# Kernel optimization log

Hardware: AMD Instinct MI355X
Metric: run time of the kernel (lower is better)

Reference implementation:

```python
import jax, jax.numpy as jnp
import numpy as np

R, STEPS, INJECT = 8, 4, 0.1


def _rmsnorm(v, w, eps=1e-6):
    return v * jax.lax.rsqrt(jnp.mean(v * v, axis=-1, keepdims=True) + eps) * w


def _layernorm(v, eps=1e-5):
    m = jnp.mean(v, axis=-1, keepdims=True)
    c = v - m
    return c * jax.lax.rsqrt(jnp.mean(c * c, axis=-1, keepdims=True) + eps)


def setup_inputs() -> dict:
    key = jax.random.key(0)
    ks = jax.random.split(key, 32)
    D, H, B, L = 1024, 256, 32, 2048
    s = 0.02
    inp = {
        'x': jax.random.normal(ks[0], (B, L, D), jnp.float32),
        'u': jax.random.uniform(ks[1], (STEPS, B, 16), jnp.float32),
        'W_e1': s * jax.random.normal(ks[2], (D, H)), 'b_e1': jnp.zeros((H,)),
        'W_e2': s * jax.random.normal(ks[3], (H, R * D)), 'b_e2': jnp.zeros((R * D,)),
        'W_ih': s * jax.random.normal(ks[4], (D + R * D, 3 * H)), 'b_ih': jnp.zeros((3 * H,)),
        'W_hh': s * jax.random.normal(ks[5], (H, 3 * H)), 'b_hh': jnp.zeros((3 * H,)),
        'ctrl_h0': jnp.zeros((H,)),
        'W_op': s * jax.random.normal(ks[6], (H, 16)), 'b_op': jnp.zeros((16,)),
        'W_src': s * jax.random.normal(ks[7], (H, R)), 'b_src': jnp.zeros((R,)),
        'W_dst': s * jax.random.normal(ks[8], (H, R)), 'b_dst': jnp.zeros((R,)),
        'W_aux': s * jax.random.normal(ks[9], (H, R)), 'b_aux': jnp.zeros((R,)),
        'W_proj': s * jax.random.normal(ks[10], (D, D)),
        'op_scale': jnp.ones((1,)),
        'Wv': s * jax.random.normal(ks[11], (D, D)), 'bv': jnp.zeros((D,)),
        'Wo': s * jax.random.normal(ks[12], (D, D)), 'bo': jnp.zeros((D,)),
        'W_d1': s * jax.random.normal(ks[13], (R * D, H)), 'b_d1': jnp.zeros((H,)),
        'W_d2': s * jax.random.normal(ks[14], (H, D)), 'b_d2': jnp.zeros((D,)),
        'norm_w': jnp.ones((D,)),
    }
    return inp


def reference(x, u, W_e1, b_e1, W_e2, b_e2, W_ih, b_ih, W_hh, b_hh, ctrl_h0,
              W_op, b_op, W_src, b_src, W_dst, b_dst, W_aux, b_aux,
              W_proj, op_scale, Wv, bv, Wo, bo, W_d1, b_d1, W_d2, b_d2, norm_w):
    B, L, D = x.shape
    pooled = x.mean(1)                                             # [B,D]
    regs = (jax.nn.gelu(pooled @ W_e1 + b_e1, approximate=False) @ W_e2 + b_e2).reshape(B, R, D)
    h = jnp.broadcast_to(ctrl_h0, (B, ctrl_h0.shape[0]))
    halt = jnp.zeros((B, 1), x.dtype)
    gumbel = -jnp.log(-jnp.log(u + 1e-20) + 1e-20)                 # [STEPS,B,16]
    op_trace = []
    for s in range(STEPS):
        ci = jnp.concatenate([pooled, regs.reshape(B, -1)], -1)    # [B, D+R*D]
        gi = ci @ W_ih + b_ih
        gh = h @ W_hh + b_hh
        ir, iz, inn = jnp.split(gi, 3, -1)
        hr, hz, hn = jnp.split(gh, 3, -1)
        r = jax.nn.sigmoid(ir + hr)
        z = jax.nn.sigmoid(iz + hz)
        n = jnp.tanh(inn + r * hn)
        h = (1.0 - z) * n + z * h                                  # GRUCell
        op_w = jax.nn.softmax(h @ W_op + b_op + gumbel[s], -1)     # gumbel-softmax, tau=1, soft
        src_w = jax.nn.softmax(h @ W_src + b_src, -1)
        dst_w = jax.nn.softmax(h @ W_dst + b_dst, -1)
        aux_w = jax.nn.softmax(h @ W_aux + b_aux, -1)
        src = jnp.einsum('br,brd->bd', src_w, regs)
        dst = jnp.einsum('br,brd->bd', dst_w, regs)
        aux = jnp.einsum('br,brd->bd', aux_w, regs)
        halt = halt + op_w[:, 15:16]
        live = jnp.clip(1.0 - halt, 0.0, None)
        # seq-len-1 MHA: softmax over one key == 1 -> out_proj(v_proj(aux))
        attn_out = (aux @ Wv + bv) @ Wo + bo
        results = jnp.stack([
            dst,                               # 0 NOP
            dst + src,                         # 1 ADD
            jax.nn.sigmoid(src) * dst,         # 2 GATE
            _layernorm(src),                   # 3 NORM
            src @ W_proj,                      # 4 PROJ
            src + dst,                         # 5 RESIDUAL
            attn_out,                          # 6 ATTEND
            -src,                              # 7 NEGATE
            src * op_scale,                    # 8 SCALE
            src,                               # 9 SWAP (as written)
            jnp.maximum(src, dst),             # 10 MAX
            jnp.minimum(src, dst),             # 11 MIN
            jax.nn.relu(src),                  # 12 RELU
            jnp.tanh(src),                     # 13 TANH
            (src * dst) @ W_proj,              # 14 OUTER
            dst,                               # 15 HALT
        ], axis=1)                             # [B,16,D]
        result = jnp.einsum('bo,bod->bd', op_w, results)
        regs = regs + dst_w[:, :, None] * (result * live)[:, None, :]
        op_trace.append(jnp.argmax(op_w, -1))
    prog_out = jax.nn.gelu(regs.reshape(B, -1) @ W_d1 + b_d1, approximate=False) @ W_d2 + b_d2
    prog_out = _rmsnorm(prog_out, norm_w)
    x_prog = _rmsnorm(x + prog_out[:, None, :] * INJECT, norm_w)
    return x_prog, regs, prog_out, jnp.stack(op_trace, axis=1)
```

## Files before the change

### kernel.cpp

```cpp
#include <hip/hip_runtime.h>
#include <math.h>
#include <stddef.h>

#define BB 32
#define LL 2048
#define DD 1024
#define HH 256
#define NSTEPS 4
#define RD 8192
#define G3 768

#define OUT_REGS 67108864UL
#define OUT_PO   67371008UL
#define OUT_TR   67403776UL

#define MM_KC 128
#define ATS 516

__device__ __forceinline__ float sigf(float x){ return 1.0f/(1.0f+expf(-x)); }
__device__ __forceinline__ float geluf(float x){ return x*0.5f*(1.0f+erff(x*0.70710678118654752f)); }

union SMem {
  struct { float At[8*ATS]; float Wt[MM_KC*64]; } mm;
  struct { float A[64*68]; float B[64*64]; } w2;
  struct { float hnew[HH]; float logit[40]; float wsm[40]; } ctl;
  struct { float ow[16]; float dw[8]; float redS[4]; float redQ[4]; float stats[2]; } comb;
  struct { float d1[HH]; float redQ[4]; float stats[1]; } dec;
};

struct MegaP {
  const float *x, *u, *W_e1, *b_e1, *W_e2, *b_e2, *W_ih, *b_ih, *W_hh, *b_hh, *h0;
  const float *W_op, *b_op, *W_src, *b_src, *W_dst, *b_dst, *W_aux, *b_aux;
  const float *W_proj, *op_sc, *Wv, *bv, *Wo, *bo, *W_d1, *b_d1, *W_d2, *b_d2, *norm_w;
  float *pool_part, *pooled, *e1, *regs, *gip_part, *gi_part, *ghpart, *hbuf, *halt;
  float *opw, *dstw, *live, *srcv, *dstv, *tvec, *avec, *p8a, *p10, *d1part, *pn;
  float *W2, *bvWo;
  float *out;
};

__device__ void st_mm2(SMem& sm, const float* __restrict__ in, int in_ld,
                       const float* __restrict__ W, int row_off, int ldw,
                       float* __restrict__ part, int nb, int layer, int nk, int t){
  float acc[16];
  #pragma unroll
  for (int i=0;i<16;++i) acc[i]=0.f;
  const int n0 = nb*64;
  for (int c=0;c<nk;++c){
    const int k0 = (layer*nk + c)*MM_KC;
    __syncthreads();
    if (t < 128){
      #pragma unroll
      for (int rep=0; rep<8; ++rep){
        int idx = t + rep*128;
        int b = idx & 31, k4 = idx >> 5;
        float4 g = *(const float4*)(in + (size_t)b*in_ld + k0 + k4*4);
        float* a = sm.mm.At + (b>>2)*ATS + k4*16 + (b&3);
        a[0]=g.x; a[4]=g.y; a[8]=g.z; a[12]=g.w;
      }
      #pragma unroll
      for (int rep=0; rep<16; ++rep){
        int idx = t + rep*128;
        int k = idx >> 4, nq4 = idx & 15;
        *(float4*)(sm.mm.Wt + k*64 + nq4*4) =
          *(const float4*)(W + (size_t)(row_off + k0 + k)*ldw + n0 + nq4*4);
      }
    }
    __syncthreads();
    if (t < 128){
      const int nq = t & 15, bq = t >> 4;
      const float4* A4 = (const float4*)sm.mm.At + bq*129;
      const float4* W4 = (const float4*)sm.mm.Wt + nq;
      #pragma unroll 4
      for (int kk=0; kk<MM_KC; ++kk){
        float4 a = A4[kk];
        float4 w = W4[kk*16];
        acc[0] +=a.x*w.x; acc[1] +=a.x*w.y; acc[2] +=a.x*w.z; acc[3] +=a.x*w.w;
        acc[4] +=a.y*w.x; acc[5] +=a.y*w.y; acc[6] +=a.y*w.z; acc[7] +=a.y*w.w;
        acc[8] +=a.z*w.x; acc[9] +=a.z*w.y; acc[10]+=a.z*w.z; acc[11]+=a.z*w.w;
        acc[12]+=a.w*w.x; acc[13]+=a.w*w.y; acc[14]+=a.w*w.z; acc[15]+=a.w*w.w;
      }
    }
  }
  if (t < 128){
    const int nq = t & 15, bq = t >> 4;
    float* pp = part + (size_t)(layer*32 + bq*4)*ldw + n0 + nq*4;
    #pragma unroll
    for (int i=0;i<4;++i){
      float4 o; o.x=acc[i*4]; o.y=acc[i*4+1]; o.z=acc[i*4+2]; o.w=acc[i*4+3];
      *(float4*)(pp + (size_t)i*ldw) = o;
    }
  }
}

__device__ void st_w2(SMem& sm, const MegaP& P, int blk, int t){
  const int r0 = (blk>>4)*64, n0 = (blk&15)*64;
  const int tr = t>>4, tc = t&15;
  float4 acc[4];
  acc[0]=make_float4(0,0,0,0); acc[1]=make_float4(0,0,0,0);
  acc[2]=make_float4(0,0,0,0); acc[3]=make_float4(0,0,0,0);
  for (int kc=0; kc<16; ++kc){
    const int k0 = kc*64;
    __syncthreads();
    #pragma unroll
    for (int rep=0; rep<4; ++rep){
      int idx = t + rep*256;
      int r = idx>>4, c4 = (idx&15)*4;
      *(float4*)(sm.w2.A + r*68 + c4) = *(const float4*)(P.Wv + (size_t)(r0+r)*DD + k0 + c4);
      *(float4*)(sm.w2.B + r*64 + c4) = *(const float4*)(P.Wo + (size_t)(k0+r)*DD + n0 + c4);
    }
    __syncthreads();
    #pragma unroll 4
    for (int k=0;k<64;++k){
      float4 bv4 = *(const float4*)(sm.w2.B + k*64 + tc*4);
      float a0 = sm.w2.A[(tr*4+0)*68 + k];
      float a1 = sm.w2.A[(tr*4+1)*68 + k];
      float a2 = sm.w2.A[(tr*4+2)*68 + k];
      float a3 = sm.w2.A[(tr*4+3)*68 + k];
      acc[0].x += a0*bv4.x; acc[0].y += a0*bv4.y; acc[0].z += a0*bv4.z; acc[0].w += a0*bv4.w;
      acc[1].x += a1*bv4.x; acc[1].y += a1*bv4.y; acc[1].z += a1*bv4.z; acc[1].w += a1*bv4.w;
      acc[2].x += a2*bv4.x; acc[2].y += a2*bv4.y; acc[2].z += a2*bv4.z; acc[2].w += a2*bv4.w;
      acc[3].x += a3*bv4.x; acc[3].y += a3*bv4.y; acc[3].z += a3*bv4.z; acc[3].w += a3*bv4.w;
    }
  }
  #pragma unroll
  for (int i=0;i<4;++i)
    *(float4*)(P.W2 + (size_t)(r0+tr*4+i)*DD + n0 + tc*4) = acc[i];
}

__global__ __launch_bounds__(256) void k_pool(MegaP P){
  const int blk = blockIdx.x, t = threadIdx.x;
  const int b = blk >> 5, c = blk & 31;
  const float* xp = P.x + (size_t)b*LL*DD + (size_t)c*64*DD + t*4;
  float ax=0.f, ay=0.f, az=0.f, aw=0.f;
  #pragma unroll 8
  for (int l=0;l<64;++l){
    float4 v = *(const float4*)(xp + (size_t)l*DD);
    ax+=v.x; ay+=v.y; az+=v.z; aw+=v.w;
  }
  float4 o; o.x=ax; o.y=ay; o.z=az; o.w=aw;
  *(float4*)(P.pool_part + (size_t)blk*DD + t*4) = o;
}

__global__ __launch_bounds__(256) void k_s1(MegaP P){
  __shared__ float pbuf[DD];
  const int blk = blockIdx.x, t = threadIdx.x;
  if (blk < 32){
    const int b = blk;
    float ax=0.f, ay=0.f, az=0.f, aw=0.f;
    #pragma unroll 8
    for (int c=0;c<32;++c){
      float4 v = *(const float4*)(P.pool_part + (size_t)(b*32+c)*DD + t*4);
      ax+=v.x; ay+=v.y; az+=v.z; aw+=v.w;
    }
    const float inv = 1.0f/(float)LL;
    float4 o; o.x=ax*inv; o.y=ay*inv; o.z=az*inv; o.w=aw*inv;
    *(float4*)(P.pooled + (size_t)b*DD + t*4) = o;
    *(float4*)(pbuf + t*4) = o;
    P.hbuf[b*HH + t] = P.h0[t];
    if (t==0) P.halt[b] = 0.f;
    __syncthreads();
    float a0=0.f,a1=0.f,a2=0.f,a3=0.f;
    #pragma unroll 2
    for (int k=0;k<DD;k+=4){
      a0 += pbuf[k]  *P.W_e1[(k)*HH + t];
      a1 += pbuf[k+1]*P.W_e1[(k+1)*HH + t];
      a2 += pbuf[k+2]*P.W_e1[(k+2)*HH + t];
      a3 += pbuf[k+3]*P.W_e1[(k+3)*HH + t];
    }
    float a = (a0+a1)+(a2+a3) + P.b_e1[t];
    P.e1[b*HH + t] = geluf(a);
  } else if (blk < 36){
    const int col = (blk-32)*256 + t;
    float a = 0.f;
    #pragma unroll 8
    for (int j=0;j<DD;++j) a += P.bv[j]*P.Wo[(size_t)j*DD + col];
    P.bvWo[col] = a;
  } else {
    const int col = (blk-36)*256 + t;
    float a = 0.f;
    #pragma unroll 8
    for (int k=0;k<HH;++k) a += P.h0[k]*P.W_hh[(size_t)k*G3 + col];
    #pragma unroll
    for (int b=0;b<BB;++b){
      P.ghpart[(size_t)b*G3 + col] = a;
      P.ghpart[(size_t)(32+b)*G3 + col] = 0.f;
    }
  }
}

__global__ __launch_bounds__(256) void k_s2(MegaP P){
  __shared__ SMem sm;
  const int blk = blockIdx.x, t = threadIdx.x;
  if (blk < 256){
    const int b = t>>3, cq = t&7;
    const int col = blk*32 + cq*4;
    float4 acc = *(const float4*)(P.b_e2 + col);
    const float* e1b = P.e1 + b*HH;
    const float* w = P.W_e2 + col;
    #pragma unroll 4
    for (int k=0;k<HH;++k){
      float ev = e1b[k];
      float4 wv = *(const float4*)(w + (size_t)k*RD);
      acc.x += ev*wv.x; acc.y += ev*wv.y; acc.z += ev*wv.z; acc.w += ev*wv.w;
    }
    *(float4*)(P.regs + (size_t)b*RD + col) = acc;
  } else if (blk < 352){
    const int i = blk - 256;
    st_mm2(sm, P.pooled, DD, P.W_ih, 0, G3, P.gip_part, i%12, i/12, 1, t);
  } else {
    st_w2(sm, P, blk-352, t);
  }
}

__global__ __launch_bounds__(128) void k_gi(MegaP P){
  __shared__ SMem sm;
  st_mm2(sm, P.regs, RD, P.W_ih, DD, G3, P.gi_part, blockIdx.x%12, blockIdx.x/12, 2, threadIdx.x);
}

__global__ __launch_bounds__(256) void k_control(MegaP P, int s){
  __shared__ SMem sm;
  const int b = blockIdx.x, t = threadIdx.x;
  const float hold = P.hbuf[b*HH + t];
  float gi[3], gh[3];
  #pragma unroll
  for (int j=0;j<3;++j){
    const int n = t + j*256;
    float a = P.b_ih[n];
    #pragma unroll
    for (int l=0;l<8;++l)  a += P.gip_part[(size_t)(l*BB+b)*G3 + n];
    #pragma unroll 8
    for (int l=0;l<32;++l) a += P.gi_part[(size_t)(l*BB+b)*G3 + n];
    gi[j] = a;
    gh[j] = P.b_hh[n] + P.ghpart[(size_t)b*G3 + n] + P.ghpart[(size_t)(32+b)*G3 + n];
  }
  {
    float r = sigf(gi[0]+gh[0]), z = sigf(gi[1]+gh[1]);
    float nn = tanhf(gi[2] + r*gh[2]);
    float hv = (1.0f - z)*nn + z*hold;
    sm.ctl.hnew[t] = hv;
    P.hbuf[b*HH + t] = hv;
  }
  __syncthreads();
  if (t < 40){
    const float* Wc; float bias; int col, ld;
    if (t < 16){ Wc=P.W_op; col=t; ld=16;
      float uu = P.u[s*BB*16 + b*16 + col];
      bias = P.b_op[col] + (-logf(-logf(uu + 1e-20f) + 1e-20f)); }
    else if (t<24){ Wc=P.W_src; col=t-16; ld=8; bias=P.b_src[col]; }
    else if (t<32){ Wc=P.W_dst; col=t-24; ld=8; bias=P.b_dst[col]; }
    else          { Wc=P.W_aux; col=t-32; ld=8; bias=P.b_aux[col]; }
    float a = bias;
    #pragma unroll 4
    for (int k=0;k<HH;++k) a += sm.ctl.hnew[k]*Wc[k*ld + col];
    sm.ctl.logit[t] = a;
  }
  __syncthreads();
  if (t == 0){
    float m = sm.ctl.logit[0]; int am = 0;
    for (int i=1;i<16;++i){ if (sm.ctl.logit[i] > m){ m = sm.ctl.logit[i]; am = i; } }
    float e[16]; float sum = 0.f;
    for (int i=0;i<16;++i){ e[i] = expf(sm.ctl.logit[i]-m); sum += e[i]; }
    float inv = 1.0f/sum;
    for (int i=0;i<16;++i){ float w = e[i]*inv; sm.ctl.wsm[i] = w; P.opw[b*16+i] = w; }
    float hl = P.halt[b] + sm.ctl.wsm[15];
    P.halt[b] = hl;
    P.live[b] = fmaxf(1.0f - hl, 0.0f);
    P.out[OUT_TR + b*NSTEPS + s] = (float)am;
  } else if (t <= 3){
    int base = 16 + (t-1)*8;
    float m = sm.ctl.logit[base];
    for (int i=1;i<8;++i) m = fmaxf(m, sm.ctl.logit[base+i]);
    float e[8]; float sum=0.f;
    for (int i=0;i<8;++i){ e[i]=expf(sm.ctl.logit[base+i]-m); sum+=e[i]; }
    float inv = 1.0f/sum;
    for (int i=0;i<8;++i){
      float w = e[i]*inv; sm.ctl.wsm[base+i] = w;
      if (t==2) P.dstw[b*8+i] = w;
    }
  }
  __syncthreads();
  {
    float w4 = sm.ctl.wsm[4], w14 = sm.ctl.wsm[14], w6 = sm.ctl.wsm[6];
    float sx=0,sy=0,sz=0,sw=0, dx=0,dy=0,dz=0,dw_=0, axx=0,ayy=0,azz=0,aww=0;
    #pragma unroll
    for (int r=0;r<8;++r){
      float ws = sm.ctl.wsm[16+r], wd = sm.ctl.wsm[24+r], wa = sm.ctl.wsm[32+r];
      float4 rv = *(const float4*)(P.regs + (size_t)b*RD + r*DD + t*4);
      sx += ws*rv.x; sy += ws*rv.y; sz += ws*rv.z; sw += ws*rv.w;
      dx += wd*rv.x; dy += wd*rv.y; dz += wd*rv.z; dw_ += wd*rv.w;
      axx += wa*rv.x; ayy += wa*rv.y; azz += wa*rv.z; aww += wa*rv.w;
    }
    float4 o;
    o.x=sx;o.y=sy;o.z=sz;o.w=sw;       *(float4*)(P.srcv + b*DD + t*4) = o;
    o.x=dx;o.y=dy;o.z=dz;o.w=dw_;      *(float4*)(P.dstv + b*DD + t*4) = o;
    o.x = w4*sx + w14*sx*dx;  o.y = w4*sy + w14*sy*dy;
    o.z = w4*sz + w14*sz*dz;  o.w = w4*sw + w14*sw*dw_;
    *(float4*)(P.tvec + b*DD + t*4) = o;
    o.x=w6*axx;o.y=w6*ayy;o.z=w6*azz;o.w=w6*aww;
    *(float4*)(P.avec + b*DD + t*4) = o;
  }
}

__global__ __launch_bounds__(128) void k_pv(MegaP P){
  __shared__ SMem sm;
  const int blk = blockIdx.x, t = threadIdx.x;
  if (blk < 128)       st_mm2(sm, P.tvec, DD, P.W_proj, 0, DD, P.p8a, blk>>3, blk&7, 1, t);
  else if (blk < 256){ int r = blk-128; st_mm2(sm, P.avec, DD, P.W2, 0, DD, P.p10, r>>3, r&7, 1, t); }
  else               { int r = blk-256; st_mm2(sm, P.hbuf, HH, P.W_hh, 0, G3, P.ghpart, r%12, r/12, 1, t); }
}

__global__ __launch_bounds__(256) void k_combine(MegaP P){
  __shared__ SMem sm;
  const int b = blockIdx.x, t = threadIdx.x;
  if (t<16) sm.comb.ow[t] = P.opw[b*16+t];
  if (t<8)  sm.comb.dw[t] = P.dstw[b*8+t];
  float4 sv = *(const float4*)(P.srcv + b*DD + t*4);
  float4 dv = *(const float4*)(P.dstv + b*DD + t*4);
  float s1 = sv.x+sv.y+sv.z+sv.w;
  float s2 = sv.x*sv.x + sv.y*sv.y + sv.z*sv.z + sv.w*sv.w;
  #pragma unroll
  for (int off=32; off; off>>=1){ s1 += __shfl_xor(s1, off, 64); s2 += __shfl_xor(s2, off, 64); }
  if ((t&63)==0){ sm.comb.redS[t>>6]=s1; sm.comb.redQ[t>>6]=s2; }
  __syncthreads();
  if (t==0){
    float S = sm.comb.redS[0]+sm.comb.redS[1]+sm.comb.redS[2]+sm.comb.redS[3];
    float Q = sm.comb.redQ[0]+sm.comb.redQ[1]+sm.comb.redQ[2]+sm.comb.redQ[3];
    float mean = S*(1.0f/DD);
    float var = Q*(1.0f/DD) - mean*mean;
    sm.comb.stats[0]=mean; sm.comb.stats[1]=rsqrtf(var + 1e-5f);
  }
  __syncthreads();
  const float mean = sm.comb.stats[0], rstd = sm.comb.stats[1];
  const float live = P.live[b], osc = P.op_sc[0];
  float pmx=0,pmy=0,pmz=0,pmw=0, atx=0,aty=0,atz=0,atw=0;
  #pragma unroll
  for (int l=0;l<8;++l){
    float4 v = *(const float4*)(P.p8a + (size_t)(l*BB+b)*DD + t*4);
    pmx+=v.x; pmy+=v.y; pmz+=v.z; pmw+=v.w;
    float4 w = *(const float4*)(P.p10 + (size_t)(l*BB+b)*DD + t*4);
    atx+=w.x; aty+=w.y; atz+=w.z; atw+=w.w;
  }
  float4 bo4 = *(const float4*)(P.bo + t*4);
  float4 bw4 = *(const float4*)(P.bvWo + t*4);
  atx += sm.comb.ow[6]*(bo4.x + bw4.x); aty += sm.comb.ow[6]*(bo4.y + bw4.y);
  atz += sm.comb.ow[6]*(bo4.z + bw4.z); atw += sm.comb.ow[6]*(bo4.w + bw4.w);
  float S[4]={sv.x,sv.y,sv.z,sv.w}, Dv[4]={dv.x,dv.y,dv.z,dv.w};
  float PM[4]={pmx,pmy,pmz,pmw}, AT[4]={atx,aty,atz,atw};
  float rl[4];
  #pragma unroll
  for (int c=0;c<4;++c){
    float sc=S[c], dc=Dv[c];
    float r = sm.comb.ow[0]*dc + sm.comb.ow[1]*(dc+sc) + sm.comb.ow[2]*(sigf(sc)*dc)
            + sm.comb.ow[3]*((sc-mean)*rstd)
            + PM[c] + sm.comb.ow[5]*(sc+dc) + AT[c]
            - sm.comb.ow[7]*sc + sm.comb.ow[8]*(sc*osc) + sm.comb.ow[9]*sc
            + sm.comb.ow[10]*fmaxf(sc,dc) + sm.comb.ow[11]*fminf(sc,dc)
            + sm.comb.ow[12]*fmaxf(sc,0.0f)
            + sm.comb.ow[13]*tanhf(sc) + sm.comb.ow[15]*dc;
    rl[c] = r*live;
  }
  #pragma unroll
  for (int r=0;r<8;++r){
    float4* rp = (float4*)(P.regs + (size_t)b*RD + r*DD + t*4);
    float4 rv = *rp;
    rv.x += sm.comb.dw[r]*rl[0]; rv.y += sm.comb.dw[r]*rl[1];
    rv.z += sm.comb.dw[r]*rl[2]; rv.w += sm.comb.dw[r]*rl[3];
    *rp = rv;
  }
}

__global__ __launch_bounds__(128) void k_d1(MegaP P){
  __shared__ SMem sm;
  st_mm2(sm, P.regs, RD, P.W_d1, 0, HH, P.d1part, blockIdx.x&3, blockIdx.x>>2, 2, threadIdx.x);
}

__global__ __launch_bounds__(256) void k_decode(MegaP P){
  __shared__ SMem sm;
  const int b = blockIdx.x, t = threadIdx.x;
  float a = P.b_d1[t];
  #pragma unroll 8
  for (int l=0;l<32;++l) a += P.d1part[(size_t)(l*BB+b)*HH + t];
  sm.dec.d1[t] = geluf(a);
  __syncthreads();
  float4 acc = *(const float4*)(P.b_d2 + t*4);
  #pragma unroll 4
  for (int k=0;k<HH;++k){
    float4 w = *(const float4*)(P.W_d2 + (size_t)k*DD + t*4);
    float dk = sm.dec.d1[k];
    acc.x += dk*w.x; acc.y += dk*w.y; acc.z += dk*w.z; acc.w += dk*w.w;
  }
  float q = acc.x*acc.x + acc.y*acc.y + acc.z*acc.z + acc.w*acc.w;
  #pragma unroll
  for (int off=32; off; off>>=1) q += __shfl_xor(q, off, 64);
  if ((t&63)==0) sm.dec.redQ[t>>6]=q;
  __syncthreads();
  if (t==0) sm.dec.stats[0] = rsqrtf((sm.dec.redQ[0]+sm.dec.redQ[1]+sm.dec.redQ[2]+sm.dec.redQ[3])*(1.0f/DD) + 1e-6f);
  __syncthreads();
  const float rs = sm.dec.stats[0];
  float4 nw = *(const float4*)(P.norm_w + t*4);
  float4 po;
  po.x = acc.x*rs*nw.x; po.y = acc.y*rs*nw.y; po.z = acc.z*rs*nw.z; po.w = acc.w*rs*nw.w;
  *(float4*)(P.pn + (size_t)b*DD + t*4) = po;
  *(float4*)(P.out + OUT_PO + (size_t)b*DD + t*4) = po;
  const float4* rsrc = (const float4*)(P.regs + (size_t)b*RD);
  float4* rdst = (float4*)(P.out + OUT_REGS + (size_t)b*RD);
  for (int i=t;i<RD/4;i+=256) rdst[i] = rsrc[i];
}

__global__ __launch_bounds__(256) void k_xprog(
    const float* __restrict__ x, const float* __restrict__ pn,
    const float* __restrict__ norm_w, float* __restrict__ out)
{
  const int t = threadIdx.x;
  const int lane = t & 63;
  const int w = blockIdx.x*4 + (t>>6);
  const int row0 = w*4;
  const int b = row0 >> 11;
  float4 nw[4], pv[4];
  #pragma unroll
  for (int j=0;j<4;++j){
    nw[j] = *(const float4*)(norm_w + j*256 + lane*4);
    float4 p = *(const float4*)(pn + (size_t)b*DD + j*256 + lane*4);
    pv[j].x = 0.1f*p.x; pv[j].y = 0.1f*p.y; pv[j].z = 0.1f*p.z; pv[j].w = 0.1f*p.w;
  }
  #pragma unroll
  for (int r=0;r<4;++r){
    const int row = row0 + r;
    const float* xp = x + (size_t)row*DD;
    float4 y[4]; float ss = 0.f;
    #pragma unroll
    for (int j=0;j<4;++j){
      float4 xv = *(const float4*)(xp + j*256 + lane*4);
      y[j].x = xv.x + pv[j].x; y[j].y = xv.y + pv[j].y;
      y[j].z = xv.z + pv[j].z; y[j].w = xv.w + pv[j].w;
      ss += y[j].x*y[j].x + y[j].y*y[j].y + y[j].z*y[j].z + y[j].w*y[j].w;
    }
    #pragma unroll
    for (int off=32; off; off>>=1) ss += __shfl_xor(ss, off, 64);
    float rsd = rsqrtf(ss*(1.0f/DD) + 1e-6f);
    float* op = out + (size_t)row*DD;
    #pragma unroll
    for (int j=0;j<4;++j){
      float4 o;
      o.x=y[j].x*rsd*nw[j].x; o.y=y[j].y*rsd*nw[j].y;
      o.z=y[j].z*rsd*nw[j].z; o.w=y[j].w*rsd*nw[j].w;
      *(float4*)(op + j*256 + lane*4) = o;
    }
  }
}

extern "C" void kernel_launch(void* const* d_in, const int* in_sizes, int n_in,
                              void* d_out, int out_size, void* d_ws, size_t ws_size,
                              hipStream_t stream)
{
  (void)in_sizes; (void)n_in; (void)out_size; (void)ws_size;
  float* out = (float*)d_out;
  float* ws  = (float*)d_ws;

  size_t o = 0;
  float* pool_part = ws + o; o += 32UL*32*1024;
  float* pooled    = ws + o; o += 32UL*1024;
  float* e1        = ws + o; o += 32UL*256;
  float* regs      = ws + o; o += 32UL*8192;
  float* gip_part  = ws + o; o += 8UL*32*768;
  float* gi_part   = ws + o; o += 32UL*32*768;
  float* ghpart    = ws + o; o += 2UL*32*768;
  float* hbuf      = ws + o; o += 32UL*256;
  float* halt      = ws + o; o += 32;
  float* opw       = ws + o; o += 32*16;
  float* dstw      = ws + o; o += 32*8;
  float* live      = ws + o; o += 32;
  float* srcv      = ws + o; o += 32UL*1024;
  float* dstv      = ws + o; o += 32UL*1024;
  float* tvec      = ws + o; o += 32UL*1024;
  float* avec      = ws + o; o += 32UL*1024;
  float* p8a       = ws + o; o += 8UL*32*1024;
  float* p10       = ws + o; o += 8UL*32*1024;
  float* d1part    = ws + o; o += 32UL*32*256;
  float* pn        = ws + o; o += 32UL*1024;
  float* W2        = ws + o; o += 1024UL*1024;
  float* bvWo      = ws + o; o += 1024;

  MegaP P;
  P.x     = (const float*)d_in[0];
  P.u     = (const float*)d_in[1];
  P.W_e1  = (const float*)d_in[2];
  P.b_e1  = (const float*)d_in[3];
  P.W_e2  = (const float*)d_in[4];
  P.b_e2  = (const float*)d_in[5];
  P.W_ih  = (const float*)d_in[6];
  P.b_ih  = (const float*)d_in[7];
  P.W_hh  = (const float*)d_in[8];
  P.b_hh  = (const float*)d_in[9];
  P.h0    = (const float*)d_in[10];
  P.W_op  = (const float*)d_in[11];
  P.b_op  = (const float*)d_in[12];
  P.W_src = (const float*)d_in[13];
  P.b_src = (const float*)d_in[14];
  P.W_dst = (const float*)d_in[15];
  P.b_dst = (const float*)d_in[16];
  P.W_aux = (const float*)d_in[17];
  P.b_aux = (const float*)d_in[18];
  P.W_proj= (const float*)d_in[19];
  P.op_sc = (const float*)d_in[20];
  P.Wv    = (const float*)d_in[21];
  P.bv    = (const float*)d_in[22];
  P.Wo    = (const float*)d_in[23];
  P.bo    = (const float*)d_in[24];
  P.W_d1  = (const float*)d_in[25];
  P.b_d1  = (const float*)d_in[26];
  P.W_d2  = (const float*)d_in[27];
  P.b_d2  = (const float*)d_in[28];
  P.norm_w= (const float*)d_in[29];
  P.pool_part=pool_part; P.pooled=pooled; P.e1=e1; P.regs=regs;
  P.gip_part=gip_part; P.gi_part=gi_part; P.ghpart=ghpart; P.hbuf=hbuf; P.halt=halt;
  P.opw=opw; P.dstw=dstw; P.live=live; P.srcv=srcv; P.dstv=dstv;
  P.tvec=tvec; P.avec=avec; P.p8a=p8a; P.p10=p10; P.d1part=d1part; P.pn=pn;
  P.W2=W2; P.bvWo=bvWo; P.out=out;

  hipLaunchKernelGGL(k_pool, dim3(1024), dim3(256), 0, stream, P);
  hipLaunchKernelGGL(k_s1,   dim3(39),   dim3(256), 0, stream, P);
  hipLaunchKernelGGL(k_s2,   dim3(608),  dim3(256), 0, stream, P);
  for (int s=0;s<NSTEPS;++s){
    hipLaunchKernelGGL(k_gi,      dim3(384), dim3(128), 0, stream, P);
    hipLaunchKernelGGL(k_control, dim3(32),  dim3(256), 0, stream, P, s);
    hipLaunchKernelGGL(k_pv,      dim3(280), dim3(128), 0, stream, P);
    hipLaunchKernelGGL(k_combine, dim3(32),  dim3(256), 0, stream, P);
  }
  hipLaunchKernelGGL(k_d1,     dim3(128), dim3(128), 0, stream, P);
  hipLaunchKernelGGL(k_decode, dim3(32),  dim3(256), 0, stream, P);
  hipLaunchKernelGGL(k_xprog,  dim3(4096),dim3(256), 0, stream, P.x, pn, P.norm_w, out);
}
```

Before: 609.2 us.

## Fuse dependent kernel pairs using atomic ticket grid barriers

Merges pool+s1, gi+control, pv+combine and d1+decode into single launches. Each fused kernel's producer blocks post an agent-scope release atomic, and the first 32 consumer blocks spin on that counter before running the dependent stage. The goal is to remove about nine kernel launch gaps and their dependency bubbles from the serial control loop. In exchange, correctness depends on all producer blocks being scheduled while consumers spin, and on a memset to reset the counters on every call. The matmul stages now run with 256-thread blocks instead of 128.

```diff
diff --git a/kernel.cpp b/kernel.cpp
--- a/kernel.cpp
+++ b/kernel.cpp
@@ -35,8 +35,22 @@
   float *pool_part, *pooled, *e1, *regs, *gip_part, *gi_part, *ghpart, *hbuf, *halt;
   float *opw, *dstw, *live, *srcv, *dstv, *tvec, *avec, *p8a, *p10, *d1part, *pn;
   float *W2, *bvWo;
+  unsigned *cnt;
   float *out;
 };
+
+__device__ __forceinline__ void ticket_post(unsigned* c){
+  __syncthreads();
+  if (threadIdx.x == 0)
+    __hip_atomic_fetch_add(c, 1u, __ATOMIC_RELEASE, __HIP_MEMORY_SCOPE_AGENT);
+}
+__device__ __forceinline__ void ticket_wait(unsigned* c, unsigned N){
+  if (threadIdx.x == 0){
+    while (__hip_atomic_load(c, __ATOMIC_ACQUIRE, __HIP_MEMORY_SCOPE_AGENT) < N)
+      __builtin_amdgcn_s_sleep(16);
+  }
+  __syncthreads();
+}
 
 __device__ void st_mm2(SMem& sm, const float* __restrict__ in, int in_ld,
                        const float* __restrict__ W, int row_off, int ldw,
@@ -127,25 +141,26 @@
     *(float4*)(P.W2 + (size_t)(r0+tr*4+i)*DD + n0 + tc*4) = acc[i];
 }
 
-__global__ __launch_bounds__(256) void k_pool(MegaP P){
-  const int blk = blockIdx.x, t = threadIdx.x;
-  const int b = blk >> 5, c = blk & 31;
-  const float* xp = P.x + (size_t)b*LL*DD + (size_t)c*64*DD + t*4;
-  float ax=0.f, ay=0.f, az=0.f, aw=0.f;
-  #pragma unroll 8
-  for (int l=0;l<64;++l){
-    float4 v = *(const float4*)(xp + (size_t)l*DD);
-    ax+=v.x; ay+=v.y; az+=v.z; aw+=v.w;
-  }
-  float4 o; o.x=ax; o.y=ay; o.z=az; o.w=aw;
-  *(float4*)(P.pool_part + (size_t)blk*DD + t*4) = o;
-}
-
-__global__ __launch_bounds__(256) void k_s1(MegaP P){
+__global__ __launch_bounds__(256) void k_pool_s1(MegaP P){
   __shared__ float pbuf[DD];
   const int blk = blockIdx.x, t = threadIdx.x;
-  if (blk < 32){
-    const int b = blk;
+  if (blk < 1024){
+    const int b = blk >> 5, c = blk & 31;
+    const float* xp = P.x + (size_t)b*LL*DD + (size_t)c*64*DD + t*4;
+    float ax=0.f, ay=0.f, az=0.f, aw=0.f;
+    #pragma unroll 8
+    for (int l=0;l<64;++l){
+      float4 v = *(const float4*)(xp + (size_t)l*DD);
+      ax+=v.x; ay+=v.y; az+=v.z; aw+=v.w;
+    }
+    float4 o; o.x=ax; o.y=ay; o.z=az; o.w=aw;
+    *(float4*)(P.pool_part + (size_t)blk*DD + t*4) = o;
+    ticket_post(P.cnt + 0);
+    return;
+  }
+  if (blk < 1056){
+    ticket_wait(P.cnt + 0, 1024u);
+    const int b = blk - 1024;
     float ax=0.f, ay=0.f, az=0.f, aw=0.f;
     #pragma unroll 8
     for (int c=0;c<32;++c){
@@ -169,14 +184,14 @@
     }
     float a = (a0+a1)+(a2+a3) + P.b_e1[t];
     P.e1[b*HH + t] = geluf(a);
-  } else if (blk < 36){
-    const int col = (blk-32)*256 + t;
+  } else if (blk < 1060){
+    const int col = (blk-1056)*256 + t;
     float a = 0.f;
     #pragma unroll 8
     for (int j=0;j<DD;++j) a += P.bv[j]*P.Wo[(size_t)j*DD + col];
     P.bvWo[col] = a;
   } else {
-    const int col = (blk-36)*256 + t;
+    const int col = (blk-1060)*256 + t;
     float a = 0.f;
     #pragma unroll 8
     for (int k=0;k<HH;++k) a += P.h0[k]*P.W_hh[(size_t)k*G3 + col];
@@ -212,14 +227,15 @@
   }
 }
 
-__global__ __launch_bounds__(128) void k_gi(MegaP P){
+__global__ __launch_bounds__(256) void k_gi_ctl(MegaP P, int s){
   __shared__ SMem sm;
-  st_mm2(sm, P.regs, RD, P.W_ih, DD, G3, P.gi_part, blockIdx.x%12, blockIdx.x/12, 2, threadIdx.x);
-}
-
-__global__ __launch_bounds__(256) void k_control(MegaP P, int s){
-  __shared__ SMem sm;
-  const int b = blockIdx.x, t = threadIdx.x;
+  const int blk = blockIdx.x, t = threadIdx.x;
+  st_mm2(sm, P.regs, RD, P.W_ih, DD, G3, P.gi_part, blk%12, blk/12, 2, t);
+  ticket_post(P.cnt + 1 + s);
+  if (blk >= 32) return;
+  ticket_wait(P.cnt + 1 + s, 384u);
+
+  const int b = blk;
   const float hold = P.hbuf[b*HH + t];
   float gi[3], gh[3];
   #pragma unroll
@@ -301,17 +317,17 @@
   }
 }
 
-__global__ __launch_bounds__(128) void k_pv(MegaP P){
+__global__ __launch_bounds__(256) void k_pv_comb(MegaP P, int s){
   __shared__ SMem sm;
   const int blk = blockIdx.x, t = threadIdx.x;
   if (blk < 128)       st_mm2(sm, P.tvec, DD, P.W_proj, 0, DD, P.p8a, blk>>3, blk&7, 1, t);
   else if (blk < 256){ int r = blk-128; st_mm2(sm, P.avec, DD, P.W2, 0, DD, P.p10, r>>3, r&7, 1, t); }
   else               { int r = blk-256; st_mm2(sm, P.hbuf, HH, P.W_hh, 0, G3, P.ghpart, r%12, r/12, 1, t); }
-}
-
-__global__ __launch_bounds__(256) void k_combine(MegaP P){
-  __shared__ SMem sm;
-  const int b = blockIdx.x, t = threadIdx.x;
+  ticket_post(P.cnt + 5 + s);
+  if (blk >= 32) return;
+  ticket_wait(P.cnt + 5 + s, 280u);
+
+  const int b = blk;
   if (t<16) sm.comb.ow[t] = P.opw[b*16+t];
   if (t<8)  sm.comb.dw[t] = P.dstw[b*8+t];
   float4 sv = *(const float4*)(P.srcv + b*DD + t*4);
@@ -369,14 +385,15 @@
   }
 }
 
-__global__ __launch_bounds__(128) void k_d1(MegaP P){
+__global__ __launch_bounds__(256) void k_d1_dec(MegaP P){
   __shared__ SMem sm;
-  st_mm2(sm, P.regs, RD, P.W_d1, 0, HH, P.d1part, blockIdx.x&3, blockIdx.x>>2, 2, threadIdx.x);
-}
-
-__global__ __launch_bounds__(256) void k_decode(MegaP P){
-  __shared__ SMem sm;
-  const int b = blockIdx.x, t = threadIdx.x;
+  const int blk = blockIdx.x, t = threadIdx.x;
+  st_mm2(sm, P.regs, RD, P.W_d1, 0, HH, P.d1part, blk&3, blk>>2, 2, t);
+  ticket_post(P.cnt + 9);
+  if (blk >= 32) return;
+  ticket_wait(P.cnt + 9, 128u);
+
+  const int b = blk;
   float a = P.b_d1[t];
   #pragma unroll 8
   for (int l=0;l<32;++l) a += P.d1part[(size_t)(l*BB+b)*HH + t];
@@ -458,6 +475,7 @@
   float* ws  = (float*)d_ws;
 
   size_t o = 0;
+  unsigned* cnt    = (unsigned*)ws; o += 64;
   float* pool_part = ws + o; o += 32UL*32*1024;
   float* pooled    = ws + o; o += 32UL*1024;
   float* e1        = ws + o; o += 32UL*256;
@@ -516,18 +534,15 @@
   P.gip_part=gip_part; P.gi_part=gi_part; P.ghpart=ghpart; P.hbuf=hbuf; P.halt=halt;
   P.opw=opw; P.dstw=dstw; P.live=live; P.srcv=srcv; P.dstv=dstv;
   P.tvec=tvec; P.avec=avec; P.p8a=p8a; P.p10=p10; P.d1part=d1part; P.pn=pn;
-  P.W2=W2; P.bvWo=bvWo; P.out=out;
-
-  hipLaunchKernelGGL(k_pool, dim3(1024), dim3(256), 0, stream, P);
-  hipLaunchKernelGGL(k_s1,   dim3(39),   dim3(256), 0, stream, P);
-  hipLaunchKernelGGL(k_s2,   dim3(608),  dim3(256), 0, stream, P);
+  P.W2=W2; P.bvWo=bvWo; P.cnt=cnt; P.out=out;
+
+  hipMemsetAsync((void*)cnt, 0, 64, stream);
+  hipLaunchKernelGGL(k_pool_s1, dim3(1063), dim3(256), 0, stream, P);
+  hipLaunchKernelGGL(k_s2,      dim3(608),  dim3(256), 0, stream, P);
   for (int s=0;s<NSTEPS;++s){
-    hipLaunchKernelGGL(k_gi,      dim3(384), dim3(128), 0, stream, P);
-    hipLaunchKernelGGL(k_control, dim3(32),  dim3(256), 0, stream, P, s);
-    hipLaunchKernelGGL(k_pv,      dim3(280), dim3(128), 0, stream, P);
-    hipLaunchKernelGGL(k_combine, dim3(32),  dim3(256), 0, stream, P);
-  }
-  hipLaunchKernelGGL(k_d1,     dim3(128), dim3(128), 0, stream, P);
-  hipLaunchKernelGGL(k_decode, dim3(32),  dim3(256), 0, stream, P);
+    hipLaunchKernelGGL(k_gi_ctl,  dim3(384), dim3(256), 0, stream, P, s);
+    hipLaunchKernelGGL(k_pv_comb, dim3(280), dim3(256), 0, stream, P, s);
+  }
+  hipLaunchKernelGGL(k_d1_dec, dim3(128), dim3(256), 0, stream, P);
   hipLaunchKernelGGL(k_xprog,  dim3(4096),dim3(256), 0, stream, P.x, pn, P.norm_w, out);
 }
```

Result: slower. 774.8 us (+27.2%).
